# Performance work log

Measured on AMD Instinct MI355X. Metric: run time of the kernel, lower is better.

## Reference

```python
import jax, jax.numpy as jnp
import numpy as np

LEAKY_SLOPE = 0.2

def setup_inputs() -> dict:
    key = jax.random.key(0)
    k1, k2, k3, k4, k5 = jax.random.split(key, 5)
    N, F_IN, H, D = 8192, 256, 4, 64
    x = jax.random.normal(k1, (N, F_IN), dtype=jnp.float32)
    adj = jax.random.randint(k2, (N, N), 0, 2, dtype=jnp.int32)
    W = jax.random.normal(k3, (F_IN, H * D), dtype=jnp.float32) * 0.05
    a_l = jax.random.normal(k4, (H, D), dtype=jnp.float32) * 0.05
    a_r = jax.random.normal(k5, (H, D), dtype=jnp.float32) * 0.05
    return {"x": x, "adj": adj, "W": W, "a_l": a_l, "a_r": a_r}

def reference(x, adj, W, a_l, a_r):
    N = x.shape[0]
    H, D = a_l.shape
    # projected node features: (N, H, D)
    h = (x @ W).reshape(N, H, D)
    score_l = jnp.einsum('nhd,hd->nh', h, a_l)  # (N, H)
    score_r = jnp.einsum('nhd,hd->nh', h, a_r)  # (N, H)
    # logits[i, j, h] = score_l[i, h] + score_r[j, h]
    logits = score_l[:, None, :] + score_r[None, :, :]
    logits = jax.nn.leaky_relu(logits, negative_slope=LEAKY_SLOPE)
    # mask: keep edge (i,j) if adj[i,j] + eye[i,j] != 0
    keep = (adj + jnp.eye(N, dtype=adj.dtype)) != 0  # (N, N)
    logits = jnp.where(keep[:, :, None], logits, -jnp.inf)
    # softmax over neighbors j (axis=1), matching torch softmax(dim=1)
    attn = jax.nn.softmax(logits, axis=1)  # (N, N, H)
    out = jnp.einsum('ijh,jhf->ihf', attn, h)  # (N, H, D)
    return out.reshape(N, H * D)  # concat=True
```

## Files before the change

### kernel.cpp

```cpp
#include <hip/hip_runtime.h>
#include <hip/hip_bf16.h>
#include <hip/hip_fp16.h>

#define N 8192
#define FIN 256
#define HD 256
#define LEAKY 0.2f

typedef short sh8 __attribute__((ext_vector_type(8)));
typedef _Float16 h8 __attribute__((ext_vector_type(8)));
typedef _Float16 h2 __attribute__((ext_vector_type(2)));
typedef float f32x4 __attribute__((ext_vector_type(4)));
typedef int   i32x4 __attribute__((ext_vector_type(4)));

__device__ __forceinline__ int pack2bf(float a, float b){
  __hip_bfloat162 t = __float22bfloat162_rn(make_float2(a, b));
  union { __hip_bfloat162 h; int i; } u;
  u.h = t;
  return u.i;
}

__device__ __forceinline__ h2 u2h2(unsigned u){ union{unsigned u; h2 h;} c; c.u=u; return c.h; }
__device__ __forceinline__ unsigned h22u(h2 h){ union{unsigned u; h2 h;} c; c.h=h; return c.u; }

__global__ void k_wt(const float* __restrict__ W, __hip_bfloat16* __restrict__ Wt){
  __shared__ float t[16][17];
  int tx = threadIdx.x, ty = threadIdx.y;
  int bx = blockIdx.x*16, by = blockIdx.y*16;
  t[ty][tx] = W[(by+ty)*HD + (bx+tx)];
  __syncthreads();
  Wt[(bx+ty)*FIN + (by+tx)] = __float2bfloat16(t[tx][ty]);
}

__global__ __launch_bounds__(256, 2) void k_h(
    const float* __restrict__ x, const __hip_bfloat16* __restrict__ Wt,
    const float* __restrict__ a_l, const float* __restrict__ a_r,
    _Float16* __restrict__ ht, float* __restrict__ El, float* __restrict__ El2,
    _Float16* __restrict__ Erh, _Float16* __restrict__ Er2h)
{
  const int lane = threadIdx.x & 63;
  const int w = threadIdx.x >> 6;
  const int r0 = lane & 15, q = lane >> 4;
  const int c0 = w*64;
  const int n0 = blockIdx.x*32;

  f32x4 acc[4][2];
  #pragma unroll
  for (int m = 0; m < 4; ++m)
    #pragma unroll
    for (int nt = 0; nt < 2; ++nt)
      acc[m][nt] = (f32x4){0.f, 0.f, 0.f, 0.f};

  for (int kb = 0; kb < 8; ++kb){
    const int k = kb*32 + q*8;
    sh8 af[4];
    #pragma unroll
    for (int m = 0; m < 4; ++m)
      af[m] = *(const sh8*)(Wt + (c0 + m*16 + r0)*FIN + k);
    #pragma unroll
    for (int nt = 0; nt < 2; ++nt){
      const float* xp = x + (n0 + nt*16 + r0)*FIN + k;
      f32x4 xl = *(const f32x4*)xp;
      f32x4 xh = *(const f32x4*)(xp + 4);
      union { sh8 s; int i[4]; } bx;
      bx.i[0] = pack2bf(xl[0], xl[1]);
      bx.i[1] = pack2bf(xl[2], xl[3]);
      bx.i[2] = pack2bf(xh[0], xh[1]);
      bx.i[3] = pack2bf(xh[2], xh[3]);
      #pragma unroll
      for (int m = 0; m < 4; ++m)
        acc[m][nt] = __builtin_amdgcn_mfma_f32_16x16x32_bf16(af[m], bx.s, acc[m][nt], 0, 0, 0);
    }
  }

  float pl[2] = {0.f, 0.f}, pr[2] = {0.f, 0.f};
  #pragma unroll
  for (int m = 0; m < 4; ++m){
    #pragma unroll
    for (int reg = 0; reg < 4; ++reg){
      const int c = c0 + m*16 + q*4 + reg;
      const float alv = a_l[c], arv = a_r[c];
      #pragma unroll
      for (int nt = 0; nt < 2; ++nt){
        float v = acc[m][nt][reg];
        ht[(size_t)c*N + (n0 + nt*16 + r0)] = (_Float16)v;
        pl[nt] += v*alv;
        pr[nt] += v*arv;
      }
    }
  }
  #pragma unroll
  for (int nt = 0; nt < 2; ++nt){
    pl[nt] += __shfl_xor(pl[nt], 16); pl[nt] += __shfl_xor(pl[nt], 32);
    pr[nt] += __shfl_xor(pr[nt], 16); pr[nt] += __shfl_xor(pr[nt], 32);
  }
  if (lane < 16){
    #pragma unroll
    for (int nt = 0; nt < 2; ++nt){
      const int n = n0 + nt*16 + r0;
      const float l = pl[nt], r = pr[nt];
      El  [w*N + n] = __expf(l);
      El2 [w*N + n] = __expf(LEAKY*l);
      Erh [w*N + n] = (_Float16)__expf(r);
      Er2h[w*N + n] = (_Float16)__expf(LEAKY*r);
    }
  }
}

__global__ __launch_bounds__(256) void k_bits(const int* __restrict__ adj,
                                              unsigned long long* __restrict__ bits)
{
  const int lane = threadIdx.x & 63;
  const int wid = (blockIdx.x*256 + threadIdx.x) >> 6;
  const int nw = (gridDim.x*256) >> 6;
  const int total = (N/64)*N;
  for (int idx = wid; idx < total; idx += nw){
    const int r = idx >> 7, c = idx & 127;
    int av = __builtin_nontemporal_load(adj + (size_t)r*N + c*64 + lane);
    unsigned long long b = __ballot(av != 0);
    if (c == (r >> 6)) b |= 1ull << (r & 63);
    if (lane == 0) bits[idx] = b;
  }
}

__device__ __forceinline__ void sub_compute(
    const char* frp, int loff, i32x4 er4, i32x4 er24,
    unsigned sw0, unsigned sw1, const h2 elh[2], const h2 el2h[2], int q,
    const h8& ones, f32x4 acc[2][4], f32x4 accz[2])
{
  h8 hf[4];
  #pragma unroll
  for (int d = 0; d < 4; ++d)
    hf[d] = *(const h8*)(frp + loff + d*1024);

  #pragma unroll
  for (int m = 0; m < 2; ++m){
    const unsigned sw = ((m == 0) ? sw0 : sw1) >> (q*8);
    unsigned fu[4];
    #pragma unroll
    for (int p = 0; p < 4; ++p){
      h2 w2 = __builtin_elementwise_max(elh[m]  * u2h2((unsigned)er4[p]),
                                        el2h[m] * u2h2((unsigned)er24[p]));
      unsigned wu = h22u(w2);
      const unsigned t = sw >> (2*p);
      wu = (t & 1u) ? wu : (wu & 0xFFFF0000u);
      wu = (t & 2u) ? wu : (wu & 0x0000FFFFu);
      fu[p] = wu;
    }
    union { h8 s; unsigned u[4]; } fa;
    fa.u[0]=fu[0]; fa.u[1]=fu[1]; fa.u[2]=fu[2]; fa.u[3]=fu[3];
    #pragma unroll
    for (int d = 0; d < 4; ++d)
      acc[m][d] = __builtin_amdgcn_mfma_f32_16x16x32_f16(fa.s, hf[d], acc[m][d], 0, 0, 0);
    accz[m] = __builtin_amdgcn_mfma_f32_16x16x32_f16(fa.s, ones, accz[m], 0, 0, 0);
  }
}

__global__ __launch_bounds__(256, 4) void k_attn(
    const unsigned* __restrict__ bits32, const _Float16* __restrict__ ht,
    const float* __restrict__ El, const float* __restrict__ El2,
    const _Float16* __restrict__ Erh, const _Float16* __restrict__ Er2h,
    float* __restrict__ part, float* __restrict__ zpart)
{
  __shared__ __align__(16) char smem[32768];
  const int b = blockIdx.x;
  const int h = b & 3, jq = (b >> 2) & 3, i128 = b >> 4;
  const int tid = threadIdx.x;
  const int lane = tid & 63;
  const int w = tid >> 6;
  const int r0 = lane & 15, q = lane >> 4;
  const int ib = i128*128 + w*32;
  const int jbase = jq * 2048;

  const _Float16* gp = ht + (size_t)(h*64 + w*16 + (lane >> 2))*N
                          + jbase + (((lane & 3) ^ ((lane >> 3) & 3))*8);
  char* lb = smem + w*1024;

  const char* frp = smem + r0*64 + ((q ^ ((r0 >> 1) & 3)) << 4);

  const float* el_ = El  + h*N + ib + r0;
  const float* el2_= El2 + h*N + ib + r0;
  h2 elh[2], el2h[2];
  #pragma unroll
  for (int m = 0; m < 2; ++m){
    _Float16 a = (_Float16)el_[m*16];
    _Float16 c = (_Float16)el2_[m*16];
    elh[m]  = (h2){a, a};
    el2h[m] = (h2){c, c};
  }
  const unsigned* bp0 = bits32 + (size_t)(ib + r0)*(N/32) + (jbase >> 5);
  const unsigned* bp1 = bp0 + 16*(N/32);
  const _Float16* erq  = Erh  + h*N + jbase + q*8;
  const _Float16* er2q = Er2h + h*N + jbase + q*8;

  union { h8 s; int i[4]; } onef;
  {
    int v = (r0 == 0) ? 0x3C003C00 : 0;
    onef.i[0]=v; onef.i[1]=v; onef.i[2]=v; onef.i[3]=v;
  }

  f32x4 acc[2][4];
  f32x4 accz[2];
  #pragma unroll
  for (int m = 0; m < 2; ++m){
    accz[m] = (f32x4){0.f,0.f,0.f,0.f};
    #pragma unroll
    for (int d = 0; d < 4; ++d)
      acc[m][d] = (f32x4){0.f,0.f,0.f,0.f};
  }

#define STAGE(bufoff, t) do { \
    const _Float16* _g = gp + (t)*128; \
    _Pragma("unroll") \
    for (int _s = 0; _s < 4; ++_s) \
      __builtin_amdgcn_global_load_lds( \
        (const __attribute__((address_space(1))) void*)(_g + _s*32), \
        (__attribute__((address_space(3))) void*)(lb + (bufoff) + _s*4096), 16, 0, 0); \
  } while(0)

  STAGE(0, 0);
  __syncthreads();

  for (int t = 0; t < 16; ++t){
    const int bo = (t & 1) ? 16384 : 0;
    const int bn = bo ^ 16384;
    const int tn = (t + 1) & 15;

    i32x4 bw0 = *(const i32x4*)(bp0 + t*4);
    i32x4 bw1 = *(const i32x4*)(bp1 + t*4);
    i32x4 er4a[4], er24a[4];
    #pragma unroll
    for (int ss = 0; ss < 4; ++ss){
      er4a[ss]  = *(const i32x4*)(erq  + t*128 + ss*32);
      er24a[ss] = *(const i32x4*)(er2q + t*128 + ss*32);
    }
    __builtin_amdgcn_sched_barrier(0);
    STAGE(bn, tn);

    #pragma unroll
    for (int ss = 0; ss < 4; ++ss)
      sub_compute(frp, bo + ss*4096, er4a[ss], er24a[ss],
                  (unsigned)bw0[ss], (unsigned)bw1[ss],
                  elh, el2h, q, onef.s, acc, accz);

    __syncthreads();
  }

  if (r0 == 0){
    #pragma unroll
    for (int m = 0; m < 2; ++m)
      #pragma unroll
      for (int reg = 0; reg < 4; ++reg)
        zpart[(jq*4 + h)*N + ib + m*16 + q*4 + reg] = accz[m][reg];
  }

  float* pp = part + (size_t)jq*N*HD + h*64 + r0;
  #pragma unroll
  for (int m = 0; m < 2; ++m)
    #pragma unroll
    for (int d = 0; d < 4; ++d)
      #pragma unroll
      for (int reg = 0; reg < 4; ++reg)
        pp[(size_t)(ib + m*16 + q*4 + reg)*HD + d*16] = acc[m][d][reg];
#undef STAGE
}

__global__ void k_out(const float* __restrict__ part, const float* __restrict__ zpart,
                      float* __restrict__ out)
{
  const int t4 = (blockIdx.x*256 + threadIdx.x) * 4;
  const int i = t4 >> 8;
  const int h = (t4 & 255) >> 6;
  f32x4 a = *(const f32x4*)(part + t4);
  f32x4 bq = *(const f32x4*)(part + (size_t)N*HD + t4);
  f32x4 c = *(const f32x4*)(part + 2*(size_t)N*HD + t4);
  f32x4 d = *(const f32x4*)(part + 3*(size_t)N*HD + t4);
  float zz = zpart[h*N + i] + zpart[(4 + h)*N + i] + zpart[(8 + h)*N + i] + zpart[(12 + h)*N + i];
  f32x4 s = (a + bq + c + d) / zz;
  *(f32x4*)(out + t4) = s;
}

extern "C" void kernel_launch(void* const* d_in, const int* in_sizes, int n_in,
                              void* d_out, int out_size, void* d_ws, size_t ws_size,
                              hipStream_t stream) {
  const float* x   = (const float*)d_in[0];
  const int*   adj = (const int*)d_in[1];
  const float* W   = (const float*)d_in[2];
  const float* a_l = (const float*)d_in[3];
  const float* a_r = (const float*)d_in[4];
  float* out = (float*)d_out;

  char* ws = (char*)d_ws;
  __hip_bfloat16* Wt = (__hip_bfloat16*)ws;
  _Float16* ht   = (_Float16*)(ws + 131072);
  float*    El   = (float*)   (ws + 4325376);
  float*    El2  = (float*)   (ws + 4456448);
  _Float16* Erh  = (_Float16*)(ws + 4587520);
  _Float16* Er2h = (_Float16*)(ws + 4653056);
  unsigned long long* bits = (unsigned long long*)(ws + 4718592);
  float*    part = (float*)   (ws + 13107200);
  float*    zpart= (float*)   (ws + 46661632);

  k_wt  <<<dim3(16,16), dim3(16,16), 0, stream>>>(W, Wt);
  k_h   <<<256, 256, 0, stream>>>(x, Wt, a_l, a_r, ht, El, El2, Erh, Er2h);
  k_bits<<<4096, 256, 0, stream>>>(adj, bits);
  k_attn<<<1024, 256, 0, stream>>>((const unsigned*)bits, ht, El, El2, Erh, Er2h, part, zpart);
  k_out <<<N*HD/1024, 256, 0, stream>>>(part, zpart, out);
}
```

Before: 486.1 us.

## Fuse bitmask build into projection kernel and share staged h tiles across 8 waves

Merges the adjacency-to-bitmask pass into the projection kernel as extra blocks, so both run in one launch and can overlap. Changes the attention kernel to 512-thread blocks covering 256 rows, with 8 waves cooperatively loading the same LDS tile of h, halving per-wave staging traffic and the number of blocks. The er loads are moved inline and the sched barrier is dropped, so load and compute scheduling is left to the compiler. The larger block may raise register pressure and cut occupancy under launch_bounds(512,4).

After: 531.7 us. +9.4%, slower.

```diff
diff --git a/kernel.cpp b/kernel.cpp
--- a/kernel.cpp
+++ b/kernel.cpp
@@ -32,12 +32,29 @@
   Wt[(bx+ty)*FIN + (by+tx)] = __float2bfloat16(t[tx][ty]);
 }
 
-__global__ __launch_bounds__(256, 2) void k_h(
+__global__ __launch_bounds__(256, 2) void k_hb(
     const float* __restrict__ x, const __hip_bfloat16* __restrict__ Wt,
     const float* __restrict__ a_l, const float* __restrict__ a_r,
+    const int* __restrict__ adj,
     _Float16* __restrict__ ht, float* __restrict__ El, float* __restrict__ El2,
-    _Float16* __restrict__ Erh, _Float16* __restrict__ Er2h)
+    _Float16* __restrict__ Erh, _Float16* __restrict__ Er2h,
+    unsigned long long* __restrict__ bits)
 {
+  if (blockIdx.x >= 256){
+    const int lane = threadIdx.x & 63;
+    const int wid = ((blockIdx.x - 256)*256 + threadIdx.x) >> 6;
+    const int nw = (4096*256) >> 6;
+    const int total = (N/64)*N;
+    for (int idx = wid; idx < total; idx += nw){
+      const int r = idx >> 7, c = idx & 127;
+      int av = __builtin_nontemporal_load(adj + (size_t)r*N + c*64 + lane);
+      unsigned long long b = __ballot(av != 0);
+      if (c == (r >> 6)) b |= 1ull << (r & 63);
+      if (lane == 0) bits[idx] = b;
+    }
+    return;
+  }
+
   const int lane = threadIdx.x & 63;
   const int w = threadIdx.x >> 6;
   const int r0 = lane & 15, q = lane >> 4;
@@ -107,22 +124,6 @@
   }
 }
 
-__global__ __launch_bounds__(256) void k_bits(const int* __restrict__ adj,
-                                              unsigned long long* __restrict__ bits)
-{
-  const int lane = threadIdx.x & 63;
-  const int wid = (blockIdx.x*256 + threadIdx.x) >> 6;
-  const int nw = (gridDim.x*256) >> 6;
-  const int total = (N/64)*N;
-  for (int idx = wid; idx < total; idx += nw){
-    const int r = idx >> 7, c = idx & 127;
-    int av = __builtin_nontemporal_load(adj + (size_t)r*N + c*64 + lane);
-    unsigned long long b = __ballot(av != 0);
-    if (c == (r >> 6)) b |= 1ull << (r & 63);
-    if (lane == 0) bits[idx] = b;
-  }
-}
-
 __device__ __forceinline__ void sub_compute(
     const char* frp, int loff, i32x4 er4, i32x4 er24,
     unsigned sw0, unsigned sw1, const h2 elh[2], const h2 el2h[2], int q,
@@ -156,7 +157,7 @@
   }
 }
 
-__global__ __launch_bounds__(256, 4) void k_attn(
+__global__ __launch_bounds__(512, 4) void k_attn(
     const unsigned* __restrict__ bits32, const _Float16* __restrict__ ht,
     const float* __restrict__ El, const float* __restrict__ El2,
     const _Float16* __restrict__ Erh, const _Float16* __restrict__ Er2h,
@@ -164,27 +165,27 @@
 {
   __shared__ __align__(16) char smem[32768];
   const int b = blockIdx.x;
-  const int h = b & 3, jq = (b >> 2) & 3, i128 = b >> 4;
+  const int h = b & 3, jq = (b >> 2) & 3, i256 = b >> 4;
   const int tid = threadIdx.x;
   const int lane = tid & 63;
   const int w = tid >> 6;
   const int r0 = lane & 15, q = lane >> 4;
-  const int ib = i128*128 + w*32;
+  const int i0 = i256*256;
+  const int ib = i0 + w*32;
   const int jbase = jq * 2048;
 
-  const _Float16* gp = ht + (size_t)(h*64 + w*16 + (lane >> 2))*N
+  const int fg = w & 3, sb = (w >> 2)*2;
+  const _Float16* gp = ht + (size_t)(h*64 + fg*16 + (lane >> 2))*N
                           + jbase + (((lane & 3) ^ ((lane >> 3) & 3))*8);
-  char* lb = smem + w*1024;
+  char* lb = smem + fg*1024;
 
   const char* frp = smem + r0*64 + ((q ^ ((r0 >> 1) & 3)) << 4);
 
-  const float* el_ = El  + h*N + ib + r0;
-  const float* el2_= El2 + h*N + ib + r0;
   h2 elh[2], el2h[2];
   #pragma unroll
   for (int m = 0; m < 2; ++m){
-    _Float16 a = (_Float16)el_[m*16];
-    _Float16 c = (_Float16)el2_[m*16];
+    _Float16 a = (_Float16)El [h*N + ib + m*16 + r0];
+    _Float16 c = (_Float16)El2[h*N + ib + m*16 + r0];
     elh[m]  = (h2){a, a};
     el2h[m] = (h2){c, c};
   }
@@ -212,10 +213,10 @@
 #define STAGE(bufoff, t) do { \
     const _Float16* _g = gp + (t)*128; \
     _Pragma("unroll") \
-    for (int _s = 0; _s < 4; ++_s) \
+    for (int _s = 0; _s < 2; ++_s) \
       __builtin_amdgcn_global_load_lds( \
-        (const __attribute__((address_space(1))) void*)(_g + _s*32), \
-        (__attribute__((address_space(3))) void*)(lb + (bufoff) + _s*4096), 16, 0, 0); \
+        (const __attribute__((address_space(1))) void*)(_g + (sb + _s)*32), \
+        (__attribute__((address_space(3))) void*)(lb + (bufoff) + (sb + _s)*4096), 16, 0, 0); \
   } while(0)
 
   STAGE(0, 0);
@@ -225,26 +226,22 @@
     const int bo = (t & 1) ? 16384 : 0;
     const int bn = bo ^ 16384;
     const int tn = (t + 1) & 15;
+    STAGE(bn, tn);
 
     i32x4 bw0 = *(const i32x4*)(bp0 + t*4);
     i32x4 bw1 = *(const i32x4*)(bp1 + t*4);
-    i32x4 er4a[4], er24a[4];
     #pragma unroll
     for (int ss = 0; ss < 4; ++ss){
-      er4a[ss]  = *(const i32x4*)(erq  + t*128 + ss*32);
-      er24a[ss] = *(const i32x4*)(er2q + t*128 + ss*32);
-    }
-    __builtin_amdgcn_sched_barrier(0);
-    STAGE(bn, tn);
-
-    #pragma unroll
-    for (int ss = 0; ss < 4; ++ss)
-      sub_compute(frp, bo + ss*4096, er4a[ss], er24a[ss],
+      i32x4 er4  = *(const i32x4*)(erq  + t*128 + ss*32);
+      i32x4 er24 = *(const i32x4*)(er2q + t*128 + ss*32);
+      sub_compute(frp, bo + ss*4096, er4, er24,
                   (unsigned)bw0[ss], (unsigned)bw1[ss],
                   elh, el2h, q, onef.s, acc, accz);
+    }
 
     __syncthreads();
   }
+#undef STAGE
 
   if (r0 == 0){
     #pragma unroll
@@ -262,7 +259,6 @@
       #pragma unroll
       for (int reg = 0; reg < 4; ++reg)
         pp[(size_t)(ib + m*16 + q*4 + reg)*HD + d*16] = acc[m][d][reg];
-#undef STAGE
 }
 
 __global__ void k_out(const float* __restrict__ part, const float* __restrict__ zpart,
@@ -301,9 +297,8 @@
   float*    part = (float*)   (ws + 13107200);
   float*    zpart= (float*)   (ws + 46661632);
 
-  k_wt  <<<dim3(16,16), dim3(16,16), 0, stream>>>(W, Wt);
-  k_h   <<<256, 256, 0, stream>>>(x, Wt, a_l, a_r, ht, El, El2, Erh, Er2h);
-  k_bits<<<4096, 256, 0, stream>>>(adj, bits);
-  k_attn<<<1024, 256, 0, stream>>>((const unsigned*)bits, ht, El, El2, Erh, Er2h, part, zpart);
+  k_wt <<<dim3(16,16), dim3(16,16), 0, stream>>>(W, Wt);
+  k_hb <<<4352, 256, 0, stream>>>(x, Wt, a_l, a_r, adj, ht, El, El2, Erh, Er2h, bits);
+  k_attn<<<512, 512, 0, stream>>>((const unsigned*)bits, ht, El, El2, Erh, Er2h, part, zpart);
   k_out <<<N*HD/1024, 256, 0, stream>>>(part, zpart, out);
 }
```
